# Kernel optimization log

Measured on AMD Instinct MI355X. Metric: run time of the kernel, lower is better.

Reference implementation:

```python
import jax, jax.numpy as jnp
from jax import lax
import numpy as np

EPS = 1e-5  # BatchNorm eps (eval mode, running stats)


def _conv(x, w, b, s, p):
    y = lax.conv_general_dilated(x, w, (s, s), ((p, p), (p, p)),
                                 dimension_numbers=('NCHW', 'OIHW', 'NCHW'))
    return y + b[None, :, None, None]


def _convT(x, w, b, s, p):
    # torch ConvTranspose2d weight layout: (in, out, kh, kw)
    wf = jnp.flip(w, (2, 3)).transpose(1, 0, 2, 3)  # -> (out, in, kh, kw), flipped
    q = w.shape[2] - 1 - p
    y = lax.conv_general_dilated(x, wf, (1, 1), ((q, q), (q, q)),
                                 lhs_dilation=(s, s),
                                 dimension_numbers=('NCHW', 'OIHW', 'NCHW'))
    return y + b[None, :, None, None]


def _bn(x, g, b, m, v):
    inv = g / jnp.sqrt(v + EPS)
    return x * inv[None, :, None, None] + (b - m * inv)[None, :, None, None]


def _forward(x, p):
    (enc_w1, enc_b1, bn1_g, bn1_b, bn1_m, bn1_v,
     enc_w2, enc_b2, bn2_g, bn2_b, bn2_m, bn2_v,
     enc_w3, enc_b3, codebook,
     dec_w1, dec_b1, dec_w2, dec_b2, dec_w3, dec_b3) = p
    # encoder
    z = _conv(x, enc_w1, enc_b1, 2, 1)
    z = jax.nn.relu(_bn(z, bn1_g, bn1_b, bn1_m, bn1_v))
    z = _conv(z, enc_w2, enc_b2, 2, 1)
    z = jax.nn.relu(_bn(z, bn2_g, bn2_b, bn2_m, bn2_v))
    z = _conv(z, enc_w3, enc_b3, 1, 1)  # (B, D, H/4, W/4)
    B, D, H4, W4 = z.shape
    # vector quantization: squared-euclidean distances via GEMM expansion
    zf = z.transpose(0, 2, 3, 1).reshape(B, H4 * W4, D)  # (B, N, D)
    d = (jnp.sum(zf * zf, axis=-1, keepdims=True)
         - 2.0 * jnp.einsum('bnd,kd->bnk', zf, codebook)
         + jnp.sum(codebook * codebook, axis=-1)[None, None, :])  # (B, N, K)
    idx = jnp.argmin(d, axis=-1)  # (B, N)
    e = codebook[idx].reshape(B, H4, W4, D).transpose(0, 3, 1, 2)  # (B, D, H/4, W/4)
    # decoder
    h = jax.nn.relu(_conv(e, dec_w1, dec_b1, 1, 1))
    h = jax.nn.relu(_convT(h, dec_w2, dec_b2, 2, 1))
    x_hat = jax.nn.sigmoid(_convT(h, dec_w3, dec_b3, 2, 1))
    return x_hat, e, idx


def setup_inputs() -> dict:
    key = jax.random.key(0)
    ks = jax.random.split(key, 10)
    L, K, D = 156, 512, 128
    B, H, W = 8, 128, 128
    r = lambda k, s, sc=0.05: jax.random.normal(k, s, dtype=jnp.float32) * sc
    return {
        'x': jax.random.uniform(ks[0], (B, L, H, W), dtype=jnp.float32),
        'enc_w1': r(ks[1], (64, L, 4, 4)), 'enc_b1': jnp.zeros((64,), jnp.float32),
        'bn1_g': jnp.ones((64,), jnp.float32), 'bn1_b': jnp.zeros((64,), jnp.float32),
        'bn1_m': jnp.zeros((64,), jnp.float32), 'bn1_v': jnp.ones((64,), jnp.float32),
        'enc_w2': r(ks[2], (128, 64, 4, 4)), 'enc_b2': jnp.zeros((128,), jnp.float32),
        'bn2_g': jnp.ones((128,), jnp.float32), 'bn2_b': jnp.zeros((128,), jnp.float32),
        'bn2_m': jnp.zeros((128,), jnp.float32), 'bn2_v': jnp.ones((128,), jnp.float32),
        'enc_w3': r(ks[3], (128, 128, 3, 3)), 'enc_b3': jnp.zeros((128,), jnp.float32),
        'codebook': jax.random.normal(ks[4], (K, D), dtype=jnp.float32),
        'dec_w1': r(ks[5], (128, D, 3, 3)), 'dec_b1': jnp.zeros((128,), jnp.float32),
        'dec_w2': r(ks[6], (128, 64, 4, 4)), 'dec_b2': jnp.zeros((64,), jnp.float32),
        'dec_w3': r(ks[7], (64, L, 4, 4)), 'dec_b3': jnp.zeros((L,), jnp.float32),
    }


def reference(x, enc_w1, enc_b1, bn1_g, bn1_b, bn1_m, bn1_v,
              enc_w2, enc_b2, bn2_g, bn2_b, bn2_m, bn2_v,
              enc_w3, enc_b3, codebook,
              dec_w1, dec_b1, dec_w2, dec_b2, dec_w3, dec_b3):
    p = (enc_w1, enc_b1, bn1_g, bn1_b, bn1_m, bn1_v,
         enc_w2, enc_b2, bn2_g, bn2_b, bn2_m, bn2_v,
         enc_w3, enc_b3, codebook,
         dec_w1, dec_b1, dec_w2, dec_b2, dec_w3, dec_b3)
    return _forward(x, p)
```

## Files before the change

### kernel.cpp

```cpp
#include <hip/hip_runtime.h>
#include <math.h>

#define BN_EPS 1e-5f

typedef __attribute__((ext_vector_type(8))) short bf16x8;
typedef __attribute__((ext_vector_type(4))) float f32x4;

__device__ __forceinline__ float sigmoidf_(float v) { return 1.0f / (1.0f + expf(-v)); }

__device__ __forceinline__ unsigned short f2bf(float f) {
    union { float f; unsigned u; } v; v.f = f;
    unsigned r = v.u + 0x7fffu + ((v.u >> 16) & 1u);
    return (unsigned short)(r >> 16);
}
__device__ __forceinline__ float bf2f(unsigned short h) {
    union { unsigned u; float f; } v; v.u = ((unsigned)h) << 16;
    return v.f;
}

__global__ __launch_bounds__(256) void conv1_k(
    const float* __restrict__ x, const float* __restrict__ wg,
    const float* __restrict__ bias,
    const float* __restrict__ bng, const float* __restrict__ bnb,
    const float* __restrict__ bnm, const float* __restrict__ bnv,
    float* __restrict__ y)
{
    __shared__ float sW[64 * 68];
    __shared__ float sX[4][4][2][66];
    const int blk = blockIdx.x;
    const int b = blk >> 6, oh = blk & 63;
    const int t = threadIdx.x;
    const int ocg = t & 15, owg = t >> 4;
    const int oc0 = ocg * 4, ow0 = owg * 4;
    const int ih0 = oh * 2 - 1;

    float acc[4][4] = {};
    const int kq = t & 63, wq = t >> 6;

    for (int ic0 = 0; ic0 < 156; ic0 += 4) {
#pragma unroll
        for (int r = 0; r < 4; ++r) {
            int q4 = wq + r * 4;
            int gb = (q4 * 4) * 2496 + ic0 * 16 + kq;
            float4 v;
            v.x = wg[gb]; v.y = wg[gb + 2496]; v.z = wg[gb + 4992]; v.w = wg[gb + 7488];
            *(float4*)&sW[kq * 68 + q4 * 4] = v;
        }
        for (int li = t; li < 2080; li += 256) {
            int q = li % 130;
            int tmp = li / 130;
            int r = tmp & 3, icl = tmp >> 2;
            int iw = q - 1, ih = ih0 + r;
            float v = 0.0f;
            if ((unsigned)ih < 128u && (unsigned)iw < 128u)
                v = x[((size_t)(b * 156 + ic0 + icl) * 128 + ih) * 128 + iw];
            sX[icl][r][(iw & 1) ? 0 : 1][(iw + 1) >> 1] = v;
        }
        __syncthreads();
#pragma unroll
        for (int icl = 0; icl < 4; ++icl) {
#pragma unroll
            for (int kh = 0; kh < 4; ++kh) {
                float x0[5], x1[5];
#pragma unroll
                for (int q = 0; q < 5; ++q) {
                    x0[q] = sX[icl][kh][0][ow0 + q];
                    x1[q] = sX[icl][kh][1][ow0 + q];
                }
                const int kb = (icl * 16 + kh * 4) * 68 + oc0;
                float w0[4], w1[4], w2[4], w3[4];
                *(float4*)w0 = *(const float4*)&sW[kb];
                *(float4*)w1 = *(const float4*)&sW[kb + 68];
                *(float4*)w2 = *(const float4*)&sW[kb + 136];
                *(float4*)w3 = *(const float4*)&sW[kb + 204];
#pragma unroll
                for (int i = 0; i < 4; ++i)
#pragma unroll
                    for (int m = 0; m < 4; ++m) {
                        acc[i][m] = fmaf(w0[i], x0[m],     acc[i][m]);
                        acc[i][m] = fmaf(w1[i], x1[m],     acc[i][m]);
                        acc[i][m] = fmaf(w2[i], x0[m + 1], acc[i][m]);
                        acc[i][m] = fmaf(w3[i], x1[m + 1], acc[i][m]);
                    }
            }
        }
        __syncthreads();
    }
#pragma unroll
    for (int i = 0; i < 4; ++i) {
        int oc = oc0 + i;
        float s = bng[oc] / sqrtf(bnv[oc] + BN_EPS);
        float o = fmaf(bias[oc], s, bnb[oc] - bnm[oc] * s);
        float4 vv;
        vv.x = fmaxf(fmaf(acc[i][0], s, o), 0.0f);
        vv.y = fmaxf(fmaf(acc[i][1], s, o), 0.0f);
        vv.z = fmaxf(fmaf(acc[i][2], s, o), 0.0f);
        vv.w = fmaxf(fmaf(acc[i][3], s, o), 0.0f);
        *(float4*)&y[((size_t)(b * 64 + oc) * 64 + oh) * 64 + ow0] = vv;
    }
}

__global__ __launch_bounds__(256) void conv2_k(
    const float* __restrict__ x, const float* __restrict__ wg,
    const float* __restrict__ bias,
    const float* __restrict__ bng, const float* __restrict__ bnb,
    const float* __restrict__ bnm, const float* __restrict__ bnv,
    float* __restrict__ y)
{
    __shared__ float sW[64 * 132];
    __shared__ float sX[4][4][2][34];
    const int blk = blockIdx.x;
    const int b = blk >> 5, oh = blk & 31;
    const int t = threadIdx.x;
    const int ocg = t & 31, owg = t >> 5;
    const int oc0 = ocg * 4, ow0 = owg * 4;
    const int ih0 = oh * 2 - 1;

    float acc[4][4] = {};
    const int kq = t & 63, wq = t >> 6;

    for (int ic0 = 0; ic0 < 64; ic0 += 4) {
#pragma unroll
        for (int r = 0; r < 8; ++r) {
            int q4 = wq + r * 4;
            int gb = (q4 * 4) * 1024 + ic0 * 16 + kq;
            float4 v;
            v.x = wg[gb]; v.y = wg[gb + 1024]; v.z = wg[gb + 2048]; v.w = wg[gb + 3072];
            *(float4*)&sW[kq * 132 + q4 * 4] = v;
        }
        for (int li = t; li < 1056; li += 256) {
            int q = li % 66;
            int tmp = li / 66;
            int r = tmp & 3, icl = tmp >> 2;
            int iw = q - 1, ih = ih0 + r;
            float v = 0.0f;
            if ((unsigned)ih < 64u && (unsigned)iw < 64u)
                v = x[((size_t)(b * 64 + ic0 + icl) * 64 + ih) * 64 + iw];
            sX[icl][r][(iw & 1) ? 0 : 1][(iw + 1) >> 1] = v;
        }
        __syncthreads();
#pragma unroll
        for (int icl = 0; icl < 4; ++icl) {
#pragma unroll
            for (int kh = 0; kh < 4; ++kh) {
                float x0[5], x1[5];
#pragma unroll
                for (int q = 0; q < 5; ++q) {
                    x0[q] = sX[icl][kh][0][ow0 + q];
                    x1[q] = sX[icl][kh][1][ow0 + q];
                }
                const int kb = (icl * 16 + kh * 4) * 132 + oc0;
                float w0[4], w1[4], w2[4], w3[4];
                *(float4*)w0 = *(const float4*)&sW[kb];
                *(float4*)w1 = *(const float4*)&sW[kb + 132];
                *(float4*)w2 = *(const float4*)&sW[kb + 264];
                *(float4*)w3 = *(const float4*)&sW[kb + 396];
#pragma unroll
                for (int i = 0; i < 4; ++i)
#pragma unroll
                    for (int m = 0; m < 4; ++m) {
                        acc[i][m] = fmaf(w0[i], x0[m],     acc[i][m]);
                        acc[i][m] = fmaf(w1[i], x1[m],     acc[i][m]);
                        acc[i][m] = fmaf(w2[i], x0[m + 1], acc[i][m]);
                        acc[i][m] = fmaf(w3[i], x1[m + 1], acc[i][m]);
                    }
            }
        }
        __syncthreads();
    }
#pragma unroll
    for (int i = 0; i < 4; ++i) {
        int oc = oc0 + i;
        float s = bng[oc] / sqrtf(bnv[oc] + BN_EPS);
        float o = fmaf(bias[oc], s, bnb[oc] - bnm[oc] * s);
        float4 vv;
        vv.x = fmaxf(fmaf(acc[i][0], s, o), 0.0f);
        vv.y = fmaxf(fmaf(acc[i][1], s, o), 0.0f);
        vv.z = fmaxf(fmaf(acc[i][2], s, o), 0.0f);
        vv.w = fmaxf(fmaf(acc[i][3], s, o), 0.0f);
        *(float4*)&y[((size_t)(b * 128 + oc) * 32 + oh) * 32 + ow0] = vv;
    }
}

template <int MODE>
__global__ __launch_bounds__(256) void conv3s1_k(
    const float* __restrict__ x, const float* __restrict__ wg,
    const float* __restrict__ bias, float* __restrict__ y)
{
    __shared__ float sW[36 * 132];
    __shared__ float sX[4][3][36];
    const int blk = blockIdx.x;
    const int b = blk >> 5, oh = blk & 31;
    const int t = threadIdx.x;
    const int ocg = t & 31, owg = t >> 5;
    const int oc0 = ocg * 4, ow0 = owg * 4;
    const int ih0 = oh - 1;

    float acc[4][4] = {};

    for (int ic0 = 0; ic0 < 128; ic0 += 4) {
        for (int task = t; task < 1152; task += 256) {
            int k = task % 36;
            int qq = task / 36;
            int gb = (qq * 4) * 1152 + ic0 * 9 + k;
            float4 v;
            v.x = wg[gb]; v.y = wg[gb + 1152]; v.z = wg[gb + 2304]; v.w = wg[gb + 3456];
            *(float4*)&sW[k * 132 + qq * 4] = v;
        }
        for (int li = t; li < 408; li += 256) {
            int q = li % 34;
            int tmp = li / 34;
            int r = tmp % 3, icl = tmp / 3;
            int iw = q - 1, ih = ih0 + r;
            float v = 0.0f;
            if ((unsigned)ih < 32u && (unsigned)iw < 32u)
                v = x[((size_t)(b * 128 + ic0 + icl) * 32 + ih) * 32 + iw];
            sX[icl][r][q] = v;
        }
        __syncthreads();
#pragma unroll
        for (int icl = 0; icl < 4; ++icl) {
#pragma unroll
            for (int kh = 0; kh < 3; ++kh) {
                float xv[6];
#pragma unroll
                for (int q = 0; q < 6; ++q) xv[q] = sX[icl][kh][ow0 + q];
                const int kb = (icl * 9 + kh * 3) * 132 + oc0;
                float w0[4], w1[4], w2[4];
                *(float4*)w0 = *(const float4*)&sW[kb];
                *(float4*)w1 = *(const float4*)&sW[kb + 132];
                *(float4*)w2 = *(const float4*)&sW[kb + 264];
#pragma unroll
                for (int i = 0; i < 4; ++i)
#pragma unroll
                    for (int m = 0; m < 4; ++m) {
                        acc[i][m] = fmaf(w0[i], xv[m],     acc[i][m]);
                        acc[i][m] = fmaf(w1[i], xv[m + 1], acc[i][m]);
                        acc[i][m] = fmaf(w2[i], xv[m + 2], acc[i][m]);
                    }
            }
        }
        __syncthreads();
    }
#pragma unroll
    for (int i = 0; i < 4; ++i) {
        int oc = oc0 + i;
        float bz = bias[oc];
        float4 vv;
        float r0 = acc[i][0] + bz, r1 = acc[i][1] + bz, r2 = acc[i][2] + bz, r3 = acc[i][3] + bz;
        if (MODE == 2) { r0 = fmaxf(r0, 0.f); r1 = fmaxf(r1, 0.f); r2 = fmaxf(r2, 0.f); r3 = fmaxf(r3, 0.f); }
        vv.x = r0; vv.y = r1; vv.z = r2; vv.w = r3;
        *(float4*)&y[((size_t)(b * 128 + oc) * 32 + oh) * 32 + ow0] = vv;
    }
}

__global__ __launch_bounds__(256) void decT2_k(
    const float* __restrict__ x, const float* __restrict__ wg,
    const float* __restrict__ bias, float* __restrict__ y)
{
    __shared__ float sW[64 * 68];
    __shared__ float sX[4][2][36];
    const int blk = blockIdx.x;
    const int b = blk >> 6, oh = blk & 63;
    const int t = threadIdx.x;
    const int ocg = t & 15, owg = t >> 4;
    const int oc0 = ocg * 4, ow0 = owg * 4;
    const int kh0 = (oh + 1) & 1;
    const int ih_a = (oh + 1 - kh0) >> 1;
    const int ih_b = ih_a - 1;

    float acc[4][4] = {};

    for (int ic0 = 0; ic0 < 128; ic0 += 4) {
        for (int r = 0; r < 16; ++r) {
            int li = t + 256 * r;
            int tap = li & 15, oc = (li >> 4) & 63, icl = li >> 10;
            sW[(icl * 16 + tap) * 68 + oc] = wg[(size_t)(ic0 + icl) * 1024 + oc * 16 + tap];
        }
        for (int li = t; li < 272; li += 256) {
            int q = li % 34;
            int tmp = li / 34;
            int r = tmp & 1, icl = tmp >> 1;
            int iw = q - 1, ih = ih_b + r;
            float v = 0.0f;
            if ((unsigned)ih < 32u && (unsigned)iw < 32u)
                v = x[((size_t)(b * 128 + ic0 + icl) * 32 + ih) * 32 + iw];
            sX[icl][r][q] = v;
        }
        __syncthreads();
#pragma unroll
        for (int icl = 0; icl < 4; ++icl) {
            float x0v[4], x1v[4];
            const int ib = ow0 >> 1;
#pragma unroll
            for (int q = 0; q < 4; ++q) { x0v[q] = sX[icl][0][ib + q]; x1v[q] = sX[icl][1][ib + q]; }
            const int kbA = (icl * 16 + kh0 * 4) * 68 + oc0;
            const int kbB = kbA + 8 * 68;
            float wA0[4], wA1[4], wA2[4], wA3[4], wB0[4], wB1[4], wB2[4], wB3[4];
            *(float4*)wA0 = *(const float4*)&sW[kbA];
            *(float4*)wA1 = *(const float4*)&sW[kbA + 68];
            *(float4*)wA2 = *(const float4*)&sW[kbA + 136];
            *(float4*)wA3 = *(const float4*)&sW[kbA + 204];
            *(float4*)wB0 = *(const float4*)&sW[kbB];
            *(float4*)wB1 = *(const float4*)&sW[kbB + 68];
            *(float4*)wB2 = *(const float4*)&sW[kbB + 136];
            *(float4*)wB3 = *(const float4*)&sW[kbB + 204];
#pragma unroll
            for (int i = 0; i < 4; ++i) {
                acc[i][0] = fmaf(wA1[i], x1v[1], acc[i][0]);
                acc[i][0] = fmaf(wA3[i], x1v[0], acc[i][0]);
                acc[i][0] = fmaf(wB1[i], x0v[1], acc[i][0]);
                acc[i][0] = fmaf(wB3[i], x0v[0], acc[i][0]);
                acc[i][1] = fmaf(wA0[i], x1v[2], acc[i][1]);
                acc[i][1] = fmaf(wA2[i], x1v[1], acc[i][1]);
                acc[i][1] = fmaf(wB0[i], x0v[2], acc[i][1]);
                acc[i][1] = fmaf(wB2[i], x0v[1], acc[i][1]);
                acc[i][2] = fmaf(wA1[i], x1v[2], acc[i][2]);
                acc[i][2] = fmaf(wA3[i], x1v[1], acc[i][2]);
                acc[i][2] = fmaf(wB1[i], x0v[2], acc[i][2]);
                acc[i][2] = fmaf(wB3[i], x0v[1], acc[i][2]);
                acc[i][3] = fmaf(wA0[i], x1v[3], acc[i][3]);
                acc[i][3] = fmaf(wA2[i], x1v[2], acc[i][3]);
                acc[i][3] = fmaf(wB0[i], x0v[3], acc[i][3]);
                acc[i][3] = fmaf(wB2[i], x0v[2], acc[i][3]);
            }
        }
        __syncthreads();
    }
#pragma unroll
    for (int i = 0; i < 4; ++i) {
        int oc = oc0 + i;
        float bz = bias[oc];
        float4 vv;
        vv.x = fmaxf(acc[i][0] + bz, 0.f);
        vv.y = fmaxf(acc[i][1] + bz, 0.f);
        vv.z = fmaxf(acc[i][2] + bz, 0.f);
        vv.w = fmaxf(acc[i][3] + bz, 0.f);
        *(float4*)&y[((size_t)(b * 64 + oc) * 64 + oh) * 64 + ow0] = vv;
    }
}

__global__ __launch_bounds__(256) void h2_cvt(
    const float* __restrict__ h2,
    unsigned short* __restrict__ ph, unsigned short* __restrict__ pl)
{
    __shared__ float sX[64 * 65];
    const int bid = blockIdx.x;
    const int b = bid / 66, hp = bid % 66;
    const bool interior = (hp >= 1 && hp <= 64);
    if (interior) {
        for (int i = threadIdx.x; i < 4096; i += 256) {
            int ic = i >> 6, w = i & 63;
            sX[ic * 65 + w] = h2[((size_t)(b * 64 + ic) * 64 + (hp - 1)) * 64 + w];
        }
    }
    __syncthreads();
    const size_t base = ((size_t)(b * 66) + hp) * 66 * 64;
    for (int i = threadIdx.x; i < 4224; i += 256) {
        int wp = i >> 6, ic = i & 63;
        float v = 0.0f;
        if (interior && wp >= 1 && wp <= 64) v = sX[ic * 65 + (wp - 1)];
        unsigned short h = f2bf(v);
        ph[base + i] = h;
        pl[base + i] = f2bf(v - bf2f(h));
    }
}

__global__ __launch_bounds__(256) void prep_w3(
    const float* __restrict__ w3,
    unsigned short* __restrict__ Bh, unsigned short* __restrict__ Bl)
{
    int id = blockIdx.x * 256 + threadIdx.x;
    if (id >= 20480) return;
    int l = id & 63;
    int nf = (id >> 6) % 10;
    int kk = (id / 640) & 7;
    int c = id / 5120;
    int rh = c >> 1, rw = c & 1;
    int n = nf * 16 + (l & 15);
    int k0 = kk * 32 + (l >> 4) * 8;
    size_t off = (size_t)id * 8;
#pragma unroll
    for (int j = 0; j < 8; ++j) {
        int k = k0 + j;
        int ic = k & 63, tau = k >> 6;
        int dh = tau >> 1, dw = tau & 1;
        int kh = 3 - rh - 2 * dh, kw = 3 - rw - 2 * dw;
        float v = (n < 156) ? w3[((size_t)(ic * 156 + n) * 4 + kh) * 4 + kw] : 0.0f;
        unsigned short h = f2bf(v);
        Bh[off + j] = h;
        Bl[off + j] = f2bf(v - bf2f(h));
    }
}

__global__ __launch_bounds__(256) void decT3_mfma(
    const unsigned short* __restrict__ ah, const unsigned short* __restrict__ al,
    const unsigned short* __restrict__ Bh, const unsigned short* __restrict__ Bl,
    const float* __restrict__ bias, float* __restrict__ y)
{
    const int bid = blockIdx.x;
    const int b = bid >> 7;
    const int q = (bid >> 1) & 63;
    const int rh = bid & 1;
    const int oh = 2 * q + rh;
    const int t = threadIdx.x;
    const int l = t & 63;
    const int wv = t >> 6;
    const int mh = wv & 1, nh = wv >> 1;
    const int mo = mh * 32;
    const int lr = l & 15;
    const int lk = l >> 4;
    const int icb0 = lk * 8;

    f32x4 acc[2][2][5] = {};

    for (int tau = 0; tau < 4; ++tau) {
        const int dh = tau >> 1, dw = tau & 1;
        const size_t rowbase = ((size_t)(b * 66) + (q + rh + dh)) * 66;
#pragma unroll
        for (int ks = 0; ks < 2; ++ks) {
            const int icb = ks * 32 + icb0;
            bf16x8 Ah[2][2], Al[2][2];
#pragma unroll
            for (int cls = 0; cls < 2; ++cls)
#pragma unroll
                for (int mf = 0; mf < 2; ++mf) {
                    const int p = mo + mf * 16 + lr;
                    const size_t off = (rowbase + (p + cls + dw)) * 64 + icb;
                    Ah[cls][mf] = *(const bf16x8*)(ah + off);
                    Al[cls][mf] = *(const bf16x8*)(al + off);
                }
            const int kk = tau * 2 + ks;
#pragma unroll
            for (int nfl = 0; nfl < 5; ++nfl) {
                const int nf = nh * 5 + nfl;
#pragma unroll
                for (int cls = 0; cls < 2; ++cls) {
                    const int c = rh * 2 + cls;
                    const size_t boff = (((size_t)(c * 8 + kk)) * 10 + nf) * 512 + l * 8;
                    bf16x8 bh = *(const bf16x8*)(Bh + boff);
                    bf16x8 bl = *(const bf16x8*)(Bl + boff);
#pragma unroll
                    for (int mf = 0; mf < 2; ++mf) {
                        acc[cls][mf][nfl] = __builtin_amdgcn_mfma_f32_16x16x32_bf16(Ah[cls][mf], bh, acc[cls][mf][nfl], 0, 0, 0);
                        acc[cls][mf][nfl] = __builtin_amdgcn_mfma_f32_16x16x32_bf16(Ah[cls][mf], bl, acc[cls][mf][nfl], 0, 0, 0);
                        acc[cls][mf][nfl] = __builtin_amdgcn_mfma_f32_16x16x32_bf16(Al[cls][mf], bh, acc[cls][mf][nfl], 0, 0, 0);
                    }
                }
            }
        }
    }

    __shared__ float sC[128 * 81];
#pragma unroll
    for (int pass = 0; pass < 2; ++pass) {
        __syncthreads();
        if (nh == pass) {
#pragma unroll
            for (int cls = 0; cls < 2; ++cls)
#pragma unroll
            for (int mf = 0; mf < 2; ++mf)
#pragma unroll
            for (int nfl = 0; nfl < 5; ++nfl) {
                const int ocl = nfl * 16 + lr;
                const int oc = nh * 80 + ocl;
                const float bz = (oc < 156) ? bias[oc] : 0.0f;
#pragma unroll
                for (int r = 0; r < 4; ++r) {
                    const int p = mo + mf * 16 + lk * 4 + r;
                    const int ow = 2 * p + cls;
                    sC[ow * 81 + ocl] = sigmoidf_(acc[cls][mf][nfl][r] + bz);
                }
            }
        }
        __syncthreads();
        const int ocbase = pass * 80;
        for (int i = t; i < 80 * 128; i += 256) {
            const int ow = i & 127, ocl = i >> 7;
            const int oc = ocbase + ocl;
            if (oc < 156)
                y[(((size_t)(b * 156 + oc)) * 128 + oh) * 128 + ow] = sC[ow * 81 + ocl];
        }
    }
}

__global__ __launch_bounds__(256) void cb_norms_k(const float* __restrict__ cb,
                                                  float* __restrict__ cbn)
{
    int k = blockIdx.x * 256 + threadIdx.x;
    if (k >= 512) return;
    const float* cp = cb + (size_t)k * 128;
    float s = 0.0f;
#pragma unroll
    for (int d = 0; d < 128; ++d) s = fmaf(cp[d], cp[d], s);
    cbn[k] = s;
}

__global__ __launch_bounds__(256) void vq_k(
    const float* __restrict__ z, const float* __restrict__ cb,
    const float* __restrict__ cbn,
    float* __restrict__ e, float* __restrict__ idxf)
{
    const int blk = blockIdx.x;
    const int b = blk >> 5;
    const int n0 = (blk & 31) << 5;
    const int t = threadIdx.x;
    const int nl = t & 31, kq = t >> 5;
    const int n = n0 + nl;

    float zr[128];
#pragma unroll
    for (int d = 0; d < 128; ++d) zr[d] = z[(size_t)(b * 128 + d) * 1024 + n];
    float zn = 0.0f;
#pragma unroll
    for (int d = 0; d < 128; ++d) zn = fmaf(zr[d], zr[d], zn);

    float best = 3.4e38f;
    int bk = kq * 64;
    for (int k = kq * 64; k < kq * 64 + 64; ++k) {
        const float4* cp = (const float4*)(cb + (size_t)k * 128);
        float dot = 0.0f;
#pragma unroll
        for (int j = 0; j < 32; ++j) {
            float4 c = cp[j];
            dot = fmaf(zr[4 * j + 0], c.x, dot);
            dot = fmaf(zr[4 * j + 1], c.y, dot);
            dot = fmaf(zr[4 * j + 2], c.z, dot);
            dot = fmaf(zr[4 * j + 3], c.w, dot);
        }
        float dist = (zn - 2.0f * dot) + cbn[k];
        if (dist < best) { best = dist; bk = k; }
    }
    __shared__ float sd[8][32];
    __shared__ int si[8][32];
    sd[kq][nl] = best;
    si[kq][nl] = bk;
    __syncthreads();
    if (t < 32) {
#pragma unroll
        for (int q = 1; q < 8; ++q) {
            float d2 = sd[q][nl];
            if (d2 < best) { best = d2; bk = si[q][nl]; }
        }
        si[0][nl] = bk;
        idxf[b * 1024 + n] = (float)bk;
    }
    __syncthreads();
    for (int li = t; li < 4096; li += 256) {
        int d = li >> 5, nn = li & 31;
        e[(size_t)(b * 128 + d) * 1024 + n0 + nn] = cb[(size_t)si[0][nn] * 128 + d];
    }
}

extern "C" void kernel_launch(void* const* d_in, const int* in_sizes, int n_in,
                              void* d_out, int out_size, void* d_ws, size_t ws_size,
                              hipStream_t stream)
{
    const float* x      = (const float*)d_in[0];
    const float* enc_w1 = (const float*)d_in[1];
    const float* enc_b1 = (const float*)d_in[2];
    const float* bn1_g  = (const float*)d_in[3];
    const float* bn1_b  = (const float*)d_in[4];
    const float* bn1_m  = (const float*)d_in[5];
    const float* bn1_v  = (const float*)d_in[6];
    const float* enc_w2 = (const float*)d_in[7];
    const float* enc_b2 = (const float*)d_in[8];
    const float* bn2_g  = (const float*)d_in[9];
    const float* bn2_b  = (const float*)d_in[10];
    const float* bn2_m  = (const float*)d_in[11];
    const float* bn2_v  = (const float*)d_in[12];
    const float* enc_w3 = (const float*)d_in[13];
    const float* enc_b3 = (const float*)d_in[14];
    const float* cb     = (const float*)d_in[15];
    const float* dec_w1 = (const float*)d_in[16];
    const float* dec_b1 = (const float*)d_in[17];
    const float* dec_w2 = (const float*)d_in[18];
    const float* dec_b2 = (const float*)d_in[19];
    const float* dec_w3 = (const float*)d_in[20];
    const float* dec_b3 = (const float*)d_in[21];

    float* ws = (float*)d_ws;
    float* z1  = ws;
    float* z2  = z1 + 2097152;
    float* z3  = z2 + 1048576;
    float* cbn = z3 + 1048576;
    float* h1  = cbn + 512;
    float* h2  = h1 + 1048576;
    unsigned short* h2p_hi = (unsigned short*)ws;
    unsigned short* h2p_lo = (unsigned short*)(ws + 1115136);
    unsigned short* B3h = (unsigned short*)(ws + 7340544);
    unsigned short* B3l = (unsigned short*)(ws + 7340544 + 81920);

    float* out   = (float*)d_out;
    float* x_hat = out;
    float* e     = out + 20447232;
    float* idxf  = e + 1048576;

    prep_w3<<<80, 256, 0, stream>>>(dec_w3, B3h, B3l);
    conv1_k<<<512, 256, 0, stream>>>(x, enc_w1, enc_b1, bn1_g, bn1_b, bn1_m, bn1_v, z1);
    conv2_k<<<256, 256, 0, stream>>>(z1, enc_w2, enc_b2, bn2_g, bn2_b, bn2_m, bn2_v, z2);
    conv3s1_k<0><<<256, 256, 0, stream>>>(z2, enc_w3, enc_b3, z3);
    cb_norms_k<<<2, 256, 0, stream>>>(cb, cbn);
    vq_k<<<256, 256, 0, stream>>>(z3, cb, cbn, e, idxf);
    conv3s1_k<2><<<256, 256, 0, stream>>>(e, dec_w1, dec_b1, h1);
    decT2_k<<<512, 256, 0, stream>>>(h1, dec_w2, dec_b2, h2);
    h2_cvt<<<528, 256, 0, stream>>>(h2, h2p_hi, h2p_lo);
    decT3_mfma<<<1024, 256, 0, stream>>>(h2p_hi, h2p_lo, B3h, B3l, dec_b3, x_hat);
}
```

Baseline: 1.078 ms.

## Move first encoder conv onto bf16 MFMA with three-way split precision

Replaces the scalar FMA implementation of the first stride-2 4x4 convolution (156->64 channels) with an implicit-GEMM MFMA kernel. Weights are pre-split into three bf16 terms by a new prep kernel, and input tiles are split the same way in shared memory. Six MFMA products per pair emulate fp32 accuracy. Results pass through shared memory for the BN/ReLU epilogue. This trades extra MFMA work, per-element conversion cost and an uncoalesced-ish epilogue store pattern for matrix-core throughput on the encoder's heaviest conv.

Result: faster. 1.029 ms (-4.5%).

```diff
diff --git a/kernel.cpp b/kernel.cpp
--- a/kernel.cpp
+++ b/kernel.cpp
@@ -18,85 +18,132 @@
     return v.f;
 }
 
-__global__ __launch_bounds__(256) void conv1_k(
-    const float* __restrict__ x, const float* __restrict__ wg,
+__global__ __launch_bounds__(256) void prep_w1(
+    const float* __restrict__ w1, unsigned short* __restrict__ Bw)
+{
+    int id = blockIdx.x * 256 + threadIdx.x;
+    if (id >= 20480) return;
+    int l = id & 63;
+    int nf = (id >> 6) & 3;
+    int kk = id >> 8;
+    int oc = nf * 16 + (l & 15);
+    int chunk = kk >> 3, j = kk & 7;
+    size_t off = (size_t)id * 8;
+#pragma unroll
+    for (int jj = 0; jj < 8; ++jj) {
+        int klocal = ((l >> 4) << 3) + jj;
+        int tap = 2 * j + (klocal >> 4);
+        int ic = chunk * 16 + (klocal & 15);
+        int kh = tap >> 2, kw = tap & 3;
+        float v = (ic < 156) ? w1[((size_t)(oc * 156 + ic) * 4 + kh) * 4 + kw] : 0.0f;
+        unsigned short b0 = f2bf(v);
+        float r1 = v - bf2f(b0);
+        unsigned short b1 = f2bf(r1);
+        unsigned short b2 = f2bf(r1 - bf2f(b1));
+        Bw[off + jj]          = b0;
+        Bw[163840 + off + jj] = b1;
+        Bw[327680 + off + jj] = b2;
+    }
+}
+
+__global__ __launch_bounds__(256) void conv1_mfma(
+    const float* __restrict__ x, const unsigned short* __restrict__ Bw,
     const float* __restrict__ bias,
     const float* __restrict__ bng, const float* __restrict__ bnb,
     const float* __restrict__ bnm, const float* __restrict__ bnv,
     float* __restrict__ y)
 {
-    __shared__ float sW[64 * 68];
-    __shared__ float sX[4][4][2][66];
+    __shared__ unsigned short sA[3][4][2][66][16];
+    __shared__ float sC[64][65];
     const int blk = blockIdx.x;
     const int b = blk >> 6, oh = blk & 63;
     const int t = threadIdx.x;
-    const int ocg = t & 15, owg = t >> 4;
-    const int oc0 = ocg * 4, ow0 = owg * 4;
-    const int ih0 = oh * 2 - 1;
-
-    float acc[4][4] = {};
-    const int kq = t & 63, wq = t >> 6;
-
-    for (int ic0 = 0; ic0 < 156; ic0 += 4) {
-#pragma unroll
-        for (int r = 0; r < 4; ++r) {
-            int q4 = wq + r * 4;
-            int gb = (q4 * 4) * 2496 + ic0 * 16 + kq;
-            float4 v;
-            v.x = wg[gb]; v.y = wg[gb + 2496]; v.z = wg[gb + 4992]; v.w = wg[gb + 7488];
-            *(float4*)&sW[kq * 68 + q4 * 4] = v;
-        }
-        for (int li = t; li < 2080; li += 256) {
-            int q = li % 130;
-            int tmp = li / 130;
-            int r = tmp & 3, icl = tmp >> 2;
-            int iw = q - 1, ih = ih0 + r;
+    const int l = t & 63, wv = t >> 6;
+    const int mh = wv & 1, nh = wv >> 1;
+    const int mo = mh * 32;
+    const int lr = l & 15, lk = l >> 4;
+    const int ih0 = 2 * oh - 1;
+    const int tap_sel = lk >> 1;
+    const int ic8 = (lk & 1) * 8;
+
+    f32x4 acc[2][2] = {};
+
+    for (int c = 0; c < 10; ++c) {
+        __syncthreads();
+#pragma unroll 1
+        for (int s = 0; s < 33; ++s) {
+            int slot = t + s * 256;
+            int idx = slot % 66;
+            int rem = slot / 66;
+            int par = rem & 1, r = (rem >> 1) & 3, il = rem >> 3;
+            int ic = c * 16 + il;
+            int iw = (par == 0) ? 2 * idx - 1 : 2 * idx;
+            int ih = ih0 + r;
             float v = 0.0f;
-            if ((unsigned)ih < 128u && (unsigned)iw < 128u)
-                v = x[((size_t)(b * 156 + ic0 + icl) * 128 + ih) * 128 + iw];
-            sX[icl][r][(iw & 1) ? 0 : 1][(iw + 1) >> 1] = v;
-        }
-        __syncthreads();
-#pragma unroll
-        for (int icl = 0; icl < 4; ++icl) {
-#pragma unroll
-            for (int kh = 0; kh < 4; ++kh) {
-                float x0[5], x1[5];
-#pragma unroll
-                for (int q = 0; q < 5; ++q) {
-                    x0[q] = sX[icl][kh][0][ow0 + q];
-                    x1[q] = sX[icl][kh][1][ow0 + q];
+            if (ic < 156 && (unsigned)ih < 128u && (unsigned)iw < 128u)
+                v = x[((size_t)(b * 156 + ic) * 128 + ih) * 128 + iw];
+            unsigned short a0 = f2bf(v);
+            float r1 = v - bf2f(a0);
+            unsigned short a1 = f2bf(r1);
+            unsigned short a2 = f2bf(r1 - bf2f(a1));
+            sA[0][r][par][idx][il] = a0;
+            sA[1][r][par][idx][il] = a1;
+            sA[2][r][par][idx][il] = a2;
+        }
+        __syncthreads();
+#pragma unroll
+        for (int j = 0; j < 8; ++j) {
+            const int tap = 2 * j + tap_sel;
+            const int r = tap >> 2, kw = tap & 3;
+            const int base = ((r * 2 + (kw & 1)) * 66 + (kw >> 1)) * 16 + ic8;
+            bf16x8 A0[2], A1[2], A2[2];
+#pragma unroll
+            for (int mf = 0; mf < 2; ++mf) {
+                const int off = base + (mo + mf * 16 + lr) * 16;
+                A0[mf] = *(const bf16x8*)&sA[0][0][0][0][off];
+                A1[mf] = *(const bf16x8*)&sA[1][0][0][0][off];
+                A2[mf] = *(const bf16x8*)&sA[2][0][0][0][off];
+            }
+            const int kk = c * 8 + j;
+#pragma unroll
+            for (int nfl = 0; nfl < 2; ++nfl) {
+                const int nf = nh * 2 + nfl;
+                const size_t boff = ((size_t)(kk * 4 + nf) * 64 + l) * 8;
+                bf16x8 B0 = *(const bf16x8*)(Bw + boff);
+                bf16x8 B1 = *(const bf16x8*)(Bw + 163840 + boff);
+                bf16x8 B2 = *(const bf16x8*)(Bw + 327680 + boff);
+#pragma unroll
+                for (int mf = 0; mf < 2; ++mf) {
+                    acc[mf][nfl] = __builtin_amdgcn_mfma_f32_16x16x32_bf16(A0[mf], B0, acc[mf][nfl], 0, 0, 0);
+                    acc[mf][nfl] = __builtin_amdgcn_mfma_f32_16x16x32_bf16(A0[mf], B1, acc[mf][nfl], 0, 0, 0);
+                    acc[mf][nfl] = __builtin_amdgcn_mfma_f32_16x16x32_bf16(A1[mf], B0, acc[mf][nfl], 0, 0, 0);
+                    acc[mf][nfl] = __builtin_amdgcn_mfma_f32_16x16x32_bf16(A1[mf], B1, acc[mf][nfl], 0, 0, 0);
+                    acc[mf][nfl] = __builtin_amdgcn_mfma_f32_16x16x32_bf16(A0[mf], B2, acc[mf][nfl], 0, 0, 0);
+                    acc[mf][nfl] = __builtin_amdgcn_mfma_f32_16x16x32_bf16(A2[mf], B0, acc[mf][nfl], 0, 0, 0);
                 }
-                const int kb = (icl * 16 + kh * 4) * 68 + oc0;
-                float w0[4], w1[4], w2[4], w3[4];
-                *(float4*)w0 = *(const float4*)&sW[kb];
-                *(float4*)w1 = *(const float4*)&sW[kb + 68];
-                *(float4*)w2 = *(const float4*)&sW[kb + 136];
-                *(float4*)w3 = *(const float4*)&sW[kb + 204];
-#pragma unroll
-                for (int i = 0; i < 4; ++i)
-#pragma unroll
-                    for (int m = 0; m < 4; ++m) {
-                        acc[i][m] = fmaf(w0[i], x0[m],     acc[i][m]);
-                        acc[i][m] = fmaf(w1[i], x1[m],     acc[i][m]);
-                        acc[i][m] = fmaf(w2[i], x0[m + 1], acc[i][m]);
-                        acc[i][m] = fmaf(w3[i], x1[m + 1], acc[i][m]);
-                    }
-            }
-        }
-        __syncthreads();
-    }
-#pragma unroll
-    for (int i = 0; i < 4; ++i) {
-        int oc = oc0 + i;
+            }
+        }
+    }
+
+    __syncthreads();
+#pragma unroll
+    for (int mf = 0; mf < 2; ++mf)
+#pragma unroll
+        for (int nfl = 0; nfl < 2; ++nfl) {
+            const int oc = nh * 32 + nfl * 16 + lr;
+#pragma unroll
+            for (int r = 0; r < 4; ++r) {
+                const int p = mo + mf * 16 + lk * 4 + r;
+                sC[p][oc] = acc[mf][nfl][r];
+            }
+        }
+    __syncthreads();
+    for (int i = t; i < 4096; i += 256) {
+        const int oc = i >> 6, ow = i & 63;
         float s = bng[oc] / sqrtf(bnv[oc] + BN_EPS);
-        float o = fmaf(bias[oc], s, bnb[oc] - bnm[oc] * s);
-        float4 vv;
-        vv.x = fmaxf(fmaf(acc[i][0], s, o), 0.0f);
-        vv.y = fmaxf(fmaf(acc[i][1], s, o), 0.0f);
-        vv.z = fmaxf(fmaf(acc[i][2], s, o), 0.0f);
-        vv.w = fmaxf(fmaf(acc[i][3], s, o), 0.0f);
-        *(float4*)&y[((size_t)(b * 64 + oc) * 64 + oh) * 64 + ow0] = vv;
+        float o = bnb[oc] - bnm[oc] * s;
+        float r = fmaxf((sC[ow][oc] + bias[oc]) * s + o, 0.0f);
+        y[((size_t)(b * 64 + oc) * 64 + oh) * 64 + ow] = r;
     }
 }
 
@@ -586,6 +633,7 @@
     float* cbn = z3 + 1048576;
     float* h1  = cbn + 512;
     float* h2  = h1 + 1048576;
+    unsigned short* Bw1 = (unsigned short*)h1;
     unsigned short* h2p_hi = (unsigned short*)ws;
     unsigned short* h2p_lo = (unsigned short*)(ws + 1115136);
     unsigned short* B3h = (unsigned short*)(ws + 7340544);
@@ -596,8 +644,9 @@
     float* e     = out + 20447232;
     float* idxf  = e + 1048576;
 
+    prep_w1<<<80, 256, 0, stream>>>(enc_w1, Bw1);
     prep_w3<<<80, 256, 0, stream>>>(dec_w3, B3h, B3l);
-    conv1_k<<<512, 256, 0, stream>>>(x, enc_w1, enc_b1, bn1_g, bn1_b, bn1_m, bn1_v, z1);
+    conv1_mfma<<<512, 256, 0, stream>>>(x, Bw1, enc_b1, bn1_g, bn1_b, bn1_m, bn1_v, z1);
     conv2_k<<<256, 256, 0, stream>>>(z1, enc_w2, enc_b2, bn2_g, bn2_b, bn2_m, bn2_v, z2);
     conv3s1_k<0><<<256, 256, 0, stream>>>(z2, enc_w3, enc_b3, z3);
     cb_norms_k<<<2, 256, 0, stream>>>(cb, cbn);
```
